# Kernel optimization log

Measured on AMD Instinct MI355X. Metric: run time of the kernel, lower is better.

The kernel has to match this reference:

```python
import jax, jax.numpy as jnp
import numpy as np

D_IN = 256
D_OUT = 256

def setup_inputs() -> dict:
    key = jax.random.key(0)
    kx, kq, kk, kv = jax.random.split(key, 4)
    x = jax.random.normal(kx, (8, D_IN, 64, 64), dtype=jnp.float32)
    s = 1.0 / np.sqrt(D_IN)
    Wq = jax.random.normal(kq, (D_OUT, D_IN), dtype=jnp.float32) * s
    Wk = jax.random.normal(kk, (D_OUT, D_IN), dtype=jnp.float32) * s
    Wv = jax.random.normal(kv, (D_OUT, D_IN), dtype=jnp.float32) * s
    return {"x": x, "Wq": Wq, "Wk": Wk, "Wv": Wv}

def reference(x, Wq, Wk, Wv):
    b, c_in, h, w = x.shape
    c = Wq.shape[0]
    # 1x1 conv == channel linear; tokens along N = h*w
    xt = x.reshape(b, c_in, h * w).transpose(0, 2, 1)      # (b, N, c_in)
    q = jnp.einsum('bnc,dc->bnd', xt, Wq)                  # (b, N, c)
    k = jnp.einsum('bnc,dc->bnd', xt, Wk)
    v = jnp.einsum('bnc,dc->bnd', xt, Wv)
    wei = jnp.einsum('bnd,bmd->bnm', q, k) / jnp.sqrt(jnp.asarray(c, x.dtype))
    wei = jax.nn.softmax(wei, axis=-1)
    out = jnp.einsum('bnm,bmd->bnd', wei, v)               # (b, N, c)
    return out.transpose(0, 2, 1).reshape(b, c, h, w)
```

## Files before the change

kernel.cpp:

```cpp
#include <hip/hip_runtime.h>

#define DIN 256
#define NTOK 4096

typedef __bf16 bf16;
typedef __bf16 bf16x8 __attribute__((ext_vector_type(8)));
typedef float floatx16 __attribute__((ext_vector_type(16)));

__device__ inline floatx16 mfma32(bf16x8 a, bf16x8 b, floatx16 c) {
    return __builtin_amdgcn_mfma_f32_32x32x16_bf16(a, b, c, 0, 0, 0);
}

__device__ inline void async16(const void* g, void* l) {
    __builtin_amdgcn_global_load_lds(
        (const __attribute__((address_space(1))) unsigned int*)g,
        (__attribute__((address_space(3))) unsigned int*)l, 16, 0, 0);
}

__global__ void convert_w(const float* __restrict__ wq, const float* __restrict__ wk,
                          const float* __restrict__ wv, bf16* __restrict__ Wb) {
    int i = blockIdx.x * 256 + threadIdx.x;
    const float* src = (i < 65536) ? wq : (i < 131072 ? wk : wv);
    Wb[i] = (bf16)src[i & 65535];
}

__global__ __launch_bounds__(256, 2) void proj_kernel(
    const float* __restrict__ x, const bf16* __restrict__ Wb,
    bf16* __restrict__ Qo, bf16* __restrict__ Ko, bf16* __restrict__ Vo)
{
    __shared__ bf16 xs[64][264];
    __shared__ bf16 wsm[64][264];

    int bid = blockIdx.x;
    int b = bid & 7, nt = bid >> 3;
    int n0 = nt * 64;
    int t = threadIdx.x;
    int lane = t & 63, w = t >> 6;
    int l32 = lane & 31, h = lane >> 5;
    int tokg = w >> 1;
    int og   = w & 1;

    {
        const float* xb = x + (size_t)b * DIN * NTOK;
#pragma unroll
        for (int it = 0; it < 16; ++it) {
            int flat = it * 256 + t;
            int c = flat >> 4;
            int nf = flat & 15;
            float4 v = *(const float4*)(xb + (size_t)c * NTOK + n0 + nf * 4);
            int nn = nf * 4;
            xs[nn + 0][c] = (bf16)v.x;
            xs[nn + 1][c] = (bf16)v.y;
            xs[nn + 2][c] = (bf16)v.z;
            xs[nn + 3][c] = (bf16)v.w;
        }
    }
    __syncthreads();

    bf16x8 xf[16];
#pragma unroll
    for (int ks = 0; ks < 16; ++ks)
        xf[ks] = *(const bf16x8*)&xs[tokg * 32 + l32][ks * 16 + h * 8];

    for (int mat = 0; mat < 3; ++mat) {
        const bf16* Wm = Wb + mat * 65536;
        for (int dg = 0; dg < 4; ++dg) {
            __syncthreads();
#pragma unroll
            for (int it = 0; it < 8; ++it) {
                int flat = it * 256 + t;
                int r = flat >> 5;
                int cs = (flat & 31) * 8;
                *(bf16x8*)&wsm[r][cs] =
                    *(const bf16x8*)(Wm + (size_t)(dg * 64 + r) * 256 + cs);
            }
            __syncthreads();

            floatx16 acc;
#pragma unroll
            for (int i = 0; i < 16; ++i) acc[i] = 0.0f;

            if (mat < 2) {
#pragma unroll
                for (int ks = 0; ks < 16; ++ks) {
                    bf16x8 wf = *(const bf16x8*)&wsm[og * 32 + l32][ks * 16 + h * 8];
                    acc = mfma32(xf[ks], wf, acc);
                }
                bf16* Out = (mat == 0 ? Qo : Ko) + (size_t)b * NTOK * DIN;
                int d = dg * 64 + og * 32 + l32;
#pragma unroll
                for (int r = 0; r < 16; ++r) {
                    int tok = n0 + tokg * 32 + (r & 3) + 8 * (r >> 2) + 4 * h;
                    Out[(size_t)tok * DIN + d] = (bf16)acc[r];
                }
            } else {
#pragma unroll
                for (int ks = 0; ks < 16; ++ks) {
                    bf16x8 wf = *(const bf16x8*)&wsm[og * 32 + l32][ks * 16 + h * 8];
                    acc = mfma32(wf, xf[ks], acc);
                }
                bf16* Out = Vo + (size_t)b * DIN * NTOK;
                int tok = n0 + tokg * 32 + l32;
#pragma unroll
                for (int r = 0; r < 16; ++r) {
                    int d = dg * 64 + og * 32 + (r & 3) + 8 * (r >> 2) + 4 * h;
                    Out[(size_t)d * NTOK + tok] = (bf16)acc[r];
                }
            }
        }
    }
}

__global__ __launch_bounds__(512, 2) void attn_kernel(
    const bf16* __restrict__ Q, const bf16* __restrict__ K,
    const bf16* __restrict__ V, float* __restrict__ out)
{
    __shared__ bf16 Ks[2][64][256];
    __shared__ bf16 Vs[2][256][64];
    __shared__ bf16 Ps[128][64];

    int bid = blockIdx.x;
    int b = bid & 7, qt = bid >> 3;
    int n0 = qt * 128;
    int t = threadIdx.x, lane = t & 63, w = t >> 6;
    int l32 = lane & 31, h = lane >> 5;
    int rowg = w >> 1, colg = w & 1;

    const bf16* Qb = Q + (size_t)b * NTOK * DIN;
    const bf16* Kb = K + (size_t)b * NTOK * DIN;
    const bf16* Vb = V + (size_t)b * DIN * NTOK;

    int koff[4], vofs[4], klds[4], vlds[4];
#pragma unroll
    for (int jj = 0; jj < 4; ++jj) {
        int q = w * 4 + jj;
        int r = q * 2 + (lane >> 5);
        int ck = (lane & 31) ^ (r & 7);
        koff[jj] = (r * 256 + ck * 8) * 2;
        klds[jj] = q * 512;
        int d = q * 8 + (lane >> 3);
        int cv = (lane & 7) ^ (d & 7);
        vofs[jj] = (d * 4096 + cv * 8) * 2;
        vlds[jj] = q * 512;
    }

    bf16x8 qf[16];
    {
        const bf16* qrow = Qb + (size_t)(n0 + rowg * 32 + l32) * DIN + h * 8;
#pragma unroll
        for (int ks = 0; ks < 16; ++ks) qf[ks] = *(const bf16x8*)(qrow + ks * 16);
    }

    floatx16 oacc[4];
#pragma unroll
    for (int dg = 0; dg < 4; ++dg)
        for (int i = 0; i < 16; ++i) oacc[dg][i] = 0.0f;
    float lsum[16];
#pragma unroll
    for (int r = 0; r < 16; ++r) lsum[r] = 0.0f;

    int krow = colg * 32 + l32, kxr = krow & 7;
    int prow = rowg * 32 + l32, pxr = l32 & 7;

#pragma unroll
    for (int jj = 0; jj < 4; ++jj) {
        async16((const char*)Kb + koff[jj], (bf16*)Ks[0] + klds[jj]);
        async16((const char*)Vb + vofs[jj], (bf16*)Vs[0] + vlds[jj]);
        async16((const char*)Kb + 32768 + koff[jj], (bf16*)Ks[1] + klds[jj]);
    }
    __syncthreads();

    {
        const bf16* Krd = (const bf16*)Ks[0] + krow * 256;
        floatx16 s;
#pragma unroll
        for (int i = 0; i < 16; ++i) s[i] = 0.0f;
#pragma unroll
        for (int ks = 0; ks < 16; ++ks) {
            bf16x8 kf = *(const bf16x8*)(Krd + (((2 * ks + h) ^ kxr) * 8));
            s = mfma32(qf[ks], kf, s);
        }
#pragma unroll
        for (int r = 0; r < 16; ++r) {
            float e = __expf(s[r] * 0.0625f);
            lsum[r] += e;
            int tokl = rowg * 32 + (r & 3) + 8 * (r >> 2) + 4 * h;
            int m = colg * 32 + l32;
            Ps[tokl][((m >> 3) ^ (tokl & 7)) * 8 + (m & 7)] = (bf16)e;
        }
    }
    __syncthreads();

#pragma unroll 2
    for (int mt = 0; mt < 64; ++mt) {
        int par = mt & 1;
        const bf16* Krd = (const bf16*)Ks[par ^ 1] + krow * 256;
        const bf16* Vrd = (const bf16*)Vs[par];
        bf16* Kwr = (bf16*)Ks[par];
        bf16* Vwr = (bf16*)Vs[par ^ 1];

        {
            int kt = (mt + 2) & 63, vt = (mt + 1) & 63;
#pragma unroll
            for (int jj = 0; jj < 4; ++jj) {
                async16((const char*)Kb + kt * 32768 + koff[jj], Kwr + klds[jj]);
                async16((const char*)Vb + vt * 128   + vofs[jj], Vwr + vlds[jj]);
            }
        }

        floatx16 s2;
#pragma unroll
        for (int i = 0; i < 16; ++i) s2[i] = 0.0f;
#pragma unroll
        for (int kst = 0; kst < 4; ++kst) {
            bf16x8 pf = *(const bf16x8*)&Ps[prow][(((kst * 2 + h) ^ pxr) * 8)];
#pragma unroll
            for (int dg = 0; dg < 4; ++dg) {
                int u = kst * 4 + dg;
                bf16x8 kf = *(const bf16x8*)(Krd + (((2 * u + h) ^ kxr) * 8));
                s2 = mfma32(qf[u], kf, s2);
                int d = colg * 128 + dg * 32 + l32;
                bf16x8 vf = *(const bf16x8*)(Vrd + d * 64 + (((kst * 2 + h) ^ (d & 7)) * 8));
                oacc[dg] = mfma32(vf, pf, oacc[dg]);
            }
        }
        __syncthreads();

#pragma unroll
        for (int r = 0; r < 16; ++r) {
            float e = __expf(s2[r] * 0.0625f);
            if (mt < 63) lsum[r] += e;
            int tokl = rowg * 32 + (r & 3) + 8 * (r >> 2) + 4 * h;
            int m = colg * 32 + l32;
            Ps[tokl][((m >> 3) ^ (tokl & 7)) * 8 + (m & 7)] = (bf16)e;
        }
        __syncthreads();
    }

#pragma unroll
    for (int r = 0; r < 16; ++r) {
        float sv = lsum[r];
        sv += __shfl_xor(sv, 1);
        sv += __shfl_xor(sv, 2);
        sv += __shfl_xor(sv, 4);
        sv += __shfl_xor(sv, 8);
        sv += __shfl_xor(sv, 16);
        lsum[r] = sv;
    }
    float* Lp = (float*)&Ks[0][0][0];
    if (l32 == 0) {
#pragma unroll
        for (int r = 0; r < 16; ++r)
            Lp[colg * 128 + rowg * 32 + (r & 3) + 8 * (r >> 2) + 4 * h] = lsum[r];
    }
    __syncthreads();

    int tok = rowg * 32 + l32;
    float rinv = 1.0f / (Lp[tok] + Lp[128 + tok]);
    float* ob = out + (size_t)b * DIN * NTOK + n0 + tok;
#pragma unroll
    for (int dg = 0; dg < 4; ++dg)
#pragma unroll
        for (int r = 0; r < 16; ++r) {
            int d = colg * 128 + dg * 32 + (r & 3) + 8 * (r >> 2) + 4 * h;
            ob[(size_t)d * NTOK] = oacc[dg][r] * rinv;
        }
}

extern "C" void kernel_launch(void* const* d_in, const int* in_sizes, int n_in,
                              void* d_out, int out_size, void* d_ws, size_t ws_size,
                              hipStream_t stream) {
    const float* x  = (const float*)d_in[0];
    const float* wq = (const float*)d_in[1];
    const float* wk = (const float*)d_in[2];
    const float* wv = (const float*)d_in[3];
    float* outf = (float*)d_out;

    char* ws = (char*)d_ws;
    bf16* Wb = (bf16*)(ws);
    bf16* Qp = (bf16*)(ws + (1u << 20));
    bf16* Kp = (bf16*)(ws + (1u << 20) + (16u << 20));
    bf16* Vp = (bf16*)(ws + (1u << 20) + (32u << 20));

    convert_w<<<768, 256, 0, stream>>>(wq, wk, wv, Wb);
    proj_kernel<<<512, 256, 0, stream>>>(x, Wb, Qp, Kp, Vp);
    attn_kernel<<<256, 512, 0, stream>>>(Qp, Kp, Vp, outf);
}
```

Baseline: 276.3 us.

## Specialize warps into QK-softmax producers and PV consumers in attention kernel

Splits the eight waves of the attention block into two roles. Four waves compute QK^T scores for two 32-token chunks each and write exp'd probabilities to shared memory. The other four waves load V tiles and accumulate P·V over a 64x128 output slab. This is meant to overlap exp/softmax work with MFMA work and to raise per-wave reuse of K and P fragments, at the cost of higher register pressure (eight accumulators, two Q fragment sets) and a two-barrier lockstep handoff that could stall either role.

```diff
diff --git a/kernel.cpp b/kernel.cpp
--- a/kernel.cpp
+++ b/kernel.cpp
@@ -124,147 +124,206 @@
     int n0 = qt * 128;
     int t = threadIdx.x, lane = t & 63, w = t >> 6;
     int l32 = lane & 31, h = lane >> 5;
-    int rowg = w >> 1, colg = w & 1;
 
     const bf16* Qb = Q + (size_t)b * NTOK * DIN;
     const bf16* Kb = K + (size_t)b * NTOK * DIN;
     const bf16* Vb = V + (size_t)b * DIN * NTOK;
-
-    int koff[4], vofs[4], klds[4], vlds[4];
-#pragma unroll
-    for (int jj = 0; jj < 4; ++jj) {
-        int q = w * 4 + jj;
-        int r = q * 2 + (lane >> 5);
-        int ck = (lane & 31) ^ (r & 7);
-        koff[jj] = (r * 256 + ck * 8) * 2;
-        klds[jj] = q * 512;
-        int d = q * 8 + (lane >> 3);
-        int cv = (lane & 7) ^ (d & 7);
-        vofs[jj] = (d * 4096 + cv * 8) * 2;
-        vlds[jj] = q * 512;
+    float* Lp = (float*)&Ks[0][0][0];
+
+    if (w < 4) {
+        int tokg = w >> 1, mg = w & 1;
+        int krow = mg * 32 + l32, kxr = l32 & 7;
+
+        int koff[8];
+#pragma unroll
+        for (int jj = 0; jj < 8; ++jj) {
+            int q = w * 8 + jj;
+            int r = q * 2 + (lane >> 5);
+            int ck = (lane & 31) ^ (r & 7);
+            koff[jj] = (r * 256 + ck * 8) * 2;
+        }
+
+        bf16x8 qf[2][16];
+#pragma unroll
+        for (int ca = 0; ca < 2; ++ca) {
+            const bf16* qrow = Qb + (size_t)(n0 + tokg * 64 + ca * 32 + l32) * DIN + h * 8;
+#pragma unroll
+            for (int ks = 0; ks < 16; ++ks) qf[ca][ks] = *(const bf16x8*)(qrow + ks * 16);
+        }
+
+        float lsum[2][16];
+#pragma unroll
+        for (int ca = 0; ca < 2; ++ca)
+            for (int r = 0; r < 16; ++r) lsum[ca][r] = 0.0f;
+
+#pragma unroll
+        for (int jj = 0; jj < 8; ++jj) {
+            async16((const char*)Kb + koff[jj], (bf16*)Ks[0] + (w * 8 + jj) * 512);
+            async16((const char*)Kb + 32768 + koff[jj], (bf16*)Ks[1] + (w * 8 + jj) * 512);
+        }
+        __syncthreads();
+
+        bf16x8 pe[2][2];
+        {
+            const bf16* Krd = (const bf16*)Ks[0] + krow * 256;
+            floatx16 sa, sb;
+#pragma unroll
+            for (int i = 0; i < 16; ++i) { sa[i] = 0.0f; sb[i] = 0.0f; }
+#pragma unroll
+            for (int ks = 0; ks < 16; ++ks) {
+                bf16x8 kf = *(const bf16x8*)(Krd + (((2 * ks + h) ^ kxr) * 8));
+                sa = mfma32(qf[0][ks], kf, sa);
+                sb = mfma32(qf[1][ks], kf, sb);
+            }
+#pragma unroll
+            for (int ca = 0; ca < 2; ++ca)
+#pragma unroll
+                for (int r = 0; r < 16; ++r) {
+                    float sv = (ca ? sb[r] : sa[r]);
+                    bf16 e = (bf16)__expf(sv * 0.0625f);
+                    pe[ca][r >> 3][r & 7] = e;
+                    lsum[ca][r] += (float)e;
+                }
+#pragma unroll
+            for (int ca = 0; ca < 2; ++ca)
+#pragma unroll
+                for (int r = 0; r < 16; ++r) {
+                    int tok = tokg * 64 + ca * 32 + (r & 3) + 8 * (r >> 2) + 4 * h;
+                    int key = (r & 3) + 4 * h;
+                    Ps[tok][((mg * 4 + (l32 >> 3)) ^ key) * 8 + (l32 & 7)] = pe[ca][r >> 3][r & 7];
+                }
+        }
+        __syncthreads();
+
+#pragma unroll 2
+        for (int mt = 0; mt < 64; ++mt) {
+            if (mt < 62) {
+                int kadd = ((mt + 2) & 63) * 32768;
+#pragma unroll
+                for (int jj = 0; jj < 8; ++jj)
+                    async16((const char*)Kb + kadd + koff[jj],
+                            (bf16*)Ks[mt & 1] + (w * 8 + jj) * 512);
+            }
+            const bf16* Krd = (const bf16*)Ks[(mt + 1) & 1] + krow * 256;
+            floatx16 sa, sb;
+#pragma unroll
+            for (int i = 0; i < 16; ++i) { sa[i] = 0.0f; sb[i] = 0.0f; }
+#pragma unroll
+            for (int ks = 0; ks < 16; ++ks) {
+                bf16x8 kf = *(const bf16x8*)(Krd + (((2 * ks + h) ^ kxr) * 8));
+                sa = mfma32(qf[0][ks], kf, sa);
+                sb = mfma32(qf[1][ks], kf, sb);
+            }
+#pragma unroll
+            for (int ca = 0; ca < 2; ++ca)
+#pragma unroll
+                for (int r = 0; r < 16; ++r) {
+                    float sv = (ca ? sb[r] : sa[r]);
+                    bf16 e = (bf16)__expf(sv * 0.0625f);
+                    pe[ca][r >> 3][r & 7] = e;
+                    if (mt < 63) lsum[ca][r] += (float)e;
+                }
+            __syncthreads();
+#pragma unroll
+            for (int ca = 0; ca < 2; ++ca)
+#pragma unroll
+                for (int r = 0; r < 16; ++r) {
+                    int tok = tokg * 64 + ca * 32 + (r & 3) + 8 * (r >> 2) + 4 * h;
+                    int key = (r & 3) + 4 * h;
+                    Ps[tok][((mg * 4 + (l32 >> 3)) ^ key) * 8 + (l32 & 7)] = pe[ca][r >> 3][r & 7];
+                }
+            __syncthreads();
+        }
+
+#pragma unroll
+        for (int ca = 0; ca < 2; ++ca)
+#pragma unroll
+            for (int r = 0; r < 16; ++r) {
+                float sv = lsum[ca][r];
+                sv += __shfl_xor(sv, 1);
+                sv += __shfl_xor(sv, 2);
+                sv += __shfl_xor(sv, 4);
+                sv += __shfl_xor(sv, 8);
+                sv += __shfl_xor(sv, 16);
+                lsum[ca][r] = sv;
+            }
+        if (l32 == 0) {
+#pragma unroll
+            for (int ca = 0; ca < 2; ++ca)
+#pragma unroll
+                for (int r = 0; r < 16; ++r)
+                    Lp[mg * 128 + tokg * 64 + ca * 32 + (r & 3) + 8 * (r >> 2) + 4 * h] = lsum[ca][r];
+        }
+        __syncthreads();
+    } else {
+        int slab = w - 4;
+        int dxr = l32 & 7, pxr = l32 & 7;
+
+        int vofs[8];
+#pragma unroll
+        for (int jj = 0; jj < 8; ++jj) {
+            int q = slab * 8 + jj;
+            int d = q * 8 + (lane >> 3);
+            int cv = (lane & 7) ^ (d & 7);
+            vofs[jj] = (d * 4096 + cv * 8) * 2;
+        }
+
+        floatx16 oacc[8];
+#pragma unroll
+        for (int i = 0; i < 8; ++i)
+            for (int j = 0; j < 16; ++j) oacc[i][j] = 0.0f;
+
+#pragma unroll
+        for (int jj = 0; jj < 8; ++jj)
+            async16((const char*)Vb + vofs[jj], (bf16*)Vs[0] + (slab * 8 + jj) * 512);
+        __syncthreads();
+        __syncthreads();
+
+#pragma unroll 2
+        for (int mt = 0; mt < 64; ++mt) {
+            if (mt < 63) {
+                int vadd = (mt + 1) * 128;
+#pragma unroll
+                for (int jj = 0; jj < 8; ++jj)
+                    async16((const char*)Vb + vadd + vofs[jj],
+                            (bf16*)Vs[(mt + 1) & 1] + (slab * 8 + jj) * 512);
+            }
+            const bf16* Vrd = (const bf16*)Vs[mt & 1];
+#pragma unroll
+            for (int kst = 0; kst < 4; ++kst) {
+                int ch = kst * 2 + h;
+                bf16x8 pb[4], va[2];
+#pragma unroll
+                for (int tc = 0; tc < 4; ++tc)
+                    pb[tc] = *(const bf16x8*)&Ps[tc * 32 + l32][((ch ^ pxr) * 8)];
+#pragma unroll
+                for (int dc = 0; dc < 2; ++dc)
+                    va[dc] = *(const bf16x8*)(Vrd + (slab * 64 + dc * 32 + l32) * 64 + ((ch ^ dxr) * 8));
+#pragma unroll
+                for (int dc = 0; dc < 2; ++dc)
+#pragma unroll
+                    for (int tc = 0; tc < 4; ++tc)
+                        oacc[dc * 4 + tc] = mfma32(va[dc], pb[tc], oacc[dc * 4 + tc]);
+            }
+            __syncthreads();
+            __syncthreads();
+        }
+
+        __syncthreads();
+        float* ob = out + (size_t)b * DIN * NTOK;
+#pragma unroll
+        for (int tc = 0; tc < 4; ++tc) {
+            int tok = tc * 32 + l32;
+            float rinv = 1.0f / (Lp[tok] + Lp[128 + tok]);
+#pragma unroll
+            for (int dc = 0; dc < 2; ++dc)
+#pragma unroll
+                for (int r = 0; r < 16; ++r) {
+                    int d = slab * 64 + dc * 32 + (r & 3) + 8 * (r >> 2) + 4 * h;
+                    ob[(size_t)d * NTOK + n0 + tok] = oacc[dc * 4 + tc][r] * rinv;
+                }
+        }
     }
-
-    bf16x8 qf[16];
-    {
-        const bf16* qrow = Qb + (size_t)(n0 + rowg * 32 + l32) * DIN + h * 8;
-#pragma unroll
-        for (int ks = 0; ks < 16; ++ks) qf[ks] = *(const bf16x8*)(qrow + ks * 16);
-    }
-
-    floatx16 oacc[4];
-#pragma unroll
-    for (int dg = 0; dg < 4; ++dg)
-        for (int i = 0; i < 16; ++i) oacc[dg][i] = 0.0f;
-    float lsum[16];
-#pragma unroll
-    for (int r = 0; r < 16; ++r) lsum[r] = 0.0f;
-
-    int krow = colg * 32 + l32, kxr = krow & 7;
-    int prow = rowg * 32 + l32, pxr = l32 & 7;
-
-#pragma unroll
-    for (int jj = 0; jj < 4; ++jj) {
-        async16((const char*)Kb + koff[jj], (bf16*)Ks[0] + klds[jj]);
-        async16((const char*)Vb + vofs[jj], (bf16*)Vs[0] + vlds[jj]);
-        async16((const char*)Kb + 32768 + koff[jj], (bf16*)Ks[1] + klds[jj]);
-    }
-    __syncthreads();
-
-    {
-        const bf16* Krd = (const bf16*)Ks[0] + krow * 256;
-        floatx16 s;
-#pragma unroll
-        for (int i = 0; i < 16; ++i) s[i] = 0.0f;
-#pragma unroll
-        for (int ks = 0; ks < 16; ++ks) {
-            bf16x8 kf = *(const bf16x8*)(Krd + (((2 * ks + h) ^ kxr) * 8));
-            s = mfma32(qf[ks], kf, s);
-        }
-#pragma unroll
-        for (int r = 0; r < 16; ++r) {
-            float e = __expf(s[r] * 0.0625f);
-            lsum[r] += e;
-            int tokl = rowg * 32 + (r & 3) + 8 * (r >> 2) + 4 * h;
-            int m = colg * 32 + l32;
-            Ps[tokl][((m >> 3) ^ (tokl & 7)) * 8 + (m & 7)] = (bf16)e;
-        }
-    }
-    __syncthreads();
-
-#pragma unroll 2
-    for (int mt = 0; mt < 64; ++mt) {
-        int par = mt & 1;
-        const bf16* Krd = (const bf16*)Ks[par ^ 1] + krow * 256;
-        const bf16* Vrd = (const bf16*)Vs[par];
-        bf16* Kwr = (bf16*)Ks[par];
-        bf16* Vwr = (bf16*)Vs[par ^ 1];
-
-        {
-            int kt = (mt + 2) & 63, vt = (mt + 1) & 63;
-#pragma unroll
-            for (int jj = 0; jj < 4; ++jj) {
-                async16((const char*)Kb + kt * 32768 + koff[jj], Kwr + klds[jj]);
-                async16((const char*)Vb + vt * 128   + vofs[jj], Vwr + vlds[jj]);
-            }
-        }
-
-        floatx16 s2;
-#pragma unroll
-        for (int i = 0; i < 16; ++i) s2[i] = 0.0f;
-#pragma unroll
-        for (int kst = 0; kst < 4; ++kst) {
-            bf16x8 pf = *(const bf16x8*)&Ps[prow][(((kst * 2 + h) ^ pxr) * 8)];
-#pragma unroll
-            for (int dg = 0; dg < 4; ++dg) {
-                int u = kst * 4 + dg;
-                bf16x8 kf = *(const bf16x8*)(Krd + (((2 * u + h) ^ kxr) * 8));
-                s2 = mfma32(qf[u], kf, s2);
-                int d = colg * 128 + dg * 32 + l32;
-                bf16x8 vf = *(const bf16x8*)(Vrd + d * 64 + (((kst * 2 + h) ^ (d & 7)) * 8));
-                oacc[dg] = mfma32(vf, pf, oacc[dg]);
-            }
-        }
-        __syncthreads();
-
-#pragma unroll
-        for (int r = 0; r < 16; ++r) {
-            float e = __expf(s2[r] * 0.0625f);
-            if (mt < 63) lsum[r] += e;
-            int tokl = rowg * 32 + (r & 3) + 8 * (r >> 2) + 4 * h;
-            int m = colg * 32 + l32;
-            Ps[tokl][((m >> 3) ^ (tokl & 7)) * 8 + (m & 7)] = (bf16)e;
-        }
-        __syncthreads();
-    }
-
-#pragma unroll
-    for (int r = 0; r < 16; ++r) {
-        float sv = lsum[r];
-        sv += __shfl_xor(sv, 1);
-        sv += __shfl_xor(sv, 2);
-        sv += __shfl_xor(sv, 4);
-        sv += __shfl_xor(sv, 8);
-        sv += __shfl_xor(sv, 16);
-        lsum[r] = sv;
-    }
-    float* Lp = (float*)&Ks[0][0][0];
-    if (l32 == 0) {
-#pragma unroll
-        for (int r = 0; r < 16; ++r)
-            Lp[colg * 128 + rowg * 32 + (r & 3) + 8 * (r >> 2) + 4 * h] = lsum[r];
-    }
-    __syncthreads();
-
-    int tok = rowg * 32 + l32;
-    float rinv = 1.0f / (Lp[tok] + Lp[128 + tok]);
-    float* ob = out + (size_t)b * DIN * NTOK + n0 + tok;
-#pragma unroll
-    for (int dg = 0; dg < 4; ++dg)
-#pragma unroll
-        for (int r = 0; r < 16; ++r) {
-            int d = colg * 128 + dg * 32 + (r & 3) + 8 * (r >> 2) + 4 * h;
-            ob[(size_t)d * NTOK] = oacc[dg][r] * rinv;
-        }
 }
 
 extern "C" void kernel_launch(void* const* d_in, const int* in_sizes, int n_in,
```

New measurement: 263.9 us. -4.5%, faster.
